# Kernel tuning notes

Measured on AMD Instinct MI355X. Metric: run time of the kernel, lower is better.

## Reference

```python
import jax, jax.numpy as jnp
import numpy as np

LOG100 = float(np.log(100.0))
EPS = 1e-12  # F.normalize eps


def _l2norm(x):
    # torch.nn.functional.normalize(x, dim=-1): x / max(||x||_2, eps)
    n = jnp.sqrt(jnp.sum(x * x, axis=-1, keepdims=True))
    return x / jnp.maximum(n, EPS)


def setup_inputs() -> dict:
    key = jax.random.key(0)
    k1, k2, k3, k4, k5 = jax.random.split(key, 5)
    B_, nH, N, d = 256, 8, 256, 64
    q = jax.random.normal(k1, (B_, nH, N, d), dtype=jnp.float32)
    k = jax.random.normal(k2, (B_, nH, N, d), dtype=jnp.float32)
    v = jax.random.normal(k3, (B_, nH, N, d), dtype=jnp.float32)
    logit_scale = jax.random.normal(k4, (nH, 1, 1), dtype=jnp.float32)
    bias = jax.random.normal(k5, (nH, N, N), dtype=jnp.float32)
    return {"q": q, "k": k, "v": v, "logit_scale": logit_scale, "bias": bias}


def reference(q, k, v, logit_scale, bias):
    B_, nH, N, d = q.shape
    # cosine-similarity attention (euclidean_dist=False branch)
    scores = jnp.einsum("bhnd,bhmd->bhnm", _l2norm(q), _l2norm(k))
    # attn_transform: Swin-v2-style clamped learned logit scale + rel-pos bias
    scale = jnp.exp(jnp.minimum(logit_scale, LOG100))  # (nH,1,1)
    scores = scores * scale[None] + bias[None]
    attn = jax.nn.softmax(scores, axis=-1)
    # attn_drop with p=0 is identity
    x = jnp.einsum("bhnm,bhmd->bhnd", attn, v)
    # reshape=True branch: x.transpose(1,2).reshape(B_, -1, H*head_dim) with H==N
    x = jnp.transpose(x, (0, 2, 1, 3)).reshape(B_, -1, N * d)  # (B_, nH, N*d)
    return x
```

## Files before the change

kernel.cpp:

```cpp
#include <hip/hip_runtime.h>

#define LOG100 4.605170185988091f
#define LOG2E  1.4426950408889634f

typedef _Float16 half8 __attribute__((ext_vector_type(8)));
typedef float f32x16 __attribute__((ext_vector_type(16)));

__global__ __launch_bounds__(256) void bias_pack(const float* __restrict__ bias,
                                                 unsigned* __restrict__ biasP) {
  __shared__ float tile[32][33];
  const int head = blockIdx.z;
  const int m0 = blockIdx.x * 32;
  const int n0 = blockIdx.y * 32;
  const float* src = bias + head * 65536;
  unsigned* dst = biasP + head * 32768;
  const int tx = threadIdx.x, ty = threadIdx.y;
#pragma unroll
  for (int i = ty; i < 32; i += 8) tile[i][tx] = src[(n0 + i) * 256 + m0 + tx];
  __syncthreads();
#pragma unroll
  for (int j = ty; j < 16; j += 8) {
    const float lo = tile[tx][2 * j] * LOG2E;
    const float hi = tile[tx][2 * j + 1] * LOG2E;
    dst[(m0 / 2 + j) * 256 + n0 + tx] =
        __builtin_bit_cast(unsigned, __builtin_amdgcn_cvt_pkrtz(lo, hi));
  }
}

template <bool USE_BT>
__global__ __launch_bounds__(512, 4) void attn_kernel(
    const float* __restrict__ q, const float* __restrict__ k, const float* __restrict__ v,
    const float* __restrict__ logit_scale, const float* __restrict__ bias,
    const unsigned* __restrict__ biasP, float* __restrict__ out) {
  __shared__ __align__(16) char smem[32768];
  _Float16* Kn = (_Float16*)smem;
  _Float16* Vt = (_Float16*)(smem + 16384);

  const int tid = threadIdx.x;
  const int wave = tid >> 6;
  const int lane = tid & 63;
  const int l31 = lane & 31;
  const int hi = lane >> 5;
  const int head = blockIdx.x;
  const int b = blockIdx.y;

  const long base = ((long)(b * 8 + head)) * (256 * 64);
  const float* qp = q + base;
  const float* kp = k + base;
  const float* vp = v + base;

  const float scale2 = __expf(fminf(logit_scale[head], LOG100)) * LOG2E;

  const int qrow = wave * 32 + l31;
  half8 qfrag[4];
  {
    float qf[4][8];
    float ssq = 0.f;
#pragma unroll
    for (int dk = 0; dk < 4; ++dk) {
      const float4 x0 = *(const float4*)(qp + qrow * 64 + dk * 16 + hi * 8);
      const float4 x1 = *(const float4*)(qp + qrow * 64 + dk * 16 + hi * 8 + 4);
      qf[dk][0] = x0.x; qf[dk][1] = x0.y; qf[dk][2] = x0.z; qf[dk][3] = x0.w;
      qf[dk][4] = x1.x; qf[dk][5] = x1.y; qf[dk][6] = x1.z; qf[dk][7] = x1.w;
      ssq += x0.x * x0.x + x0.y * x0.y + x0.z * x0.z + x0.w * x0.w;
      ssq += x1.x * x1.x + x1.y * x1.y + x1.z * x1.z + x1.w * x1.w;
    }
    ssq += __shfl_xor(ssq, 32);
    const float qinv = rsqrtf(fmaxf(ssq, 1e-24f));
#pragma unroll
    for (int dk = 0; dk < 4; ++dk)
#pragma unroll
      for (int j = 0; j < 8; ++j) qfrag[dk][j] = (_Float16)(qf[dk][j] * qinv);
  }

  f32x16 o0 = {};
  f32x16 o1 = {};
  float m = -1.0e30f, lsum = 0.f;

  const unsigned* bP = USE_BT ? (biasP + head * 32768 + qrow) : nullptr;
  const float* bF = USE_BT ? nullptr : (bias + head * 65536 + qrow * 256 + 4 * hi);

  for (int h = 0; h < 2; ++h) {
    if (h) __syncthreads();

    {
      const int row_in = tid >> 4;
      const int seg = tid & 15;
#pragma unroll
      for (int it = 0; it < 4; ++it) {
        const int r = it * 32 + row_in;
        const float4 a = *(const float4*)(kp + (h * 128 + r) * 64 + seg * 4);
        float ss = a.x * a.x + a.y * a.y + a.z * a.z + a.w * a.w;
        ss += __shfl_xor(ss, 1);
        ss += __shfl_xor(ss, 2);
        ss += __shfl_xor(ss, 4);
        ss += __shfl_xor(ss, 8);
        const float inv = rsqrtf(fmaxf(ss, 1e-24f));
        union { _Float16 hh[4]; uint2 u; } pk4;
        pk4.hh[0] = (_Float16)(a.x * inv);
        pk4.hh[1] = (_Float16)(a.y * inv);
        pk4.hh[2] = (_Float16)(a.z * inv);
        pk4.hh[3] = (_Float16)(a.w * inv);
        char* wp = (char*)Kn + r * 128 + ((seg * 8) ^ ((r & 15) << 3));
        *(uint2*)wp = pk4.u;
      }
    }

    {
      const int r = lane >> 4;
      const int sx = lane & 15;
#pragma unroll
      for (int it = 0; it < 4; ++it) {
        const int kv0 = (wave * 4 + it) * 4;
        float4 a = *(const float4*)(vp + (h * 128 + kv0 + r) * 64 + sx * 4);
        float e1 = (r & 1) ? a.x : a.y;
        float g1 = __shfl_xor(e1, 16);
        float e2 = (r & 1) ? a.z : a.w;
        float g2 = __shfl_xor(e2, 16);
        if (r & 1) { a.x = g1; a.z = g2; } else { a.y = g1; a.w = g2; }
        float e3 = (r & 2) ? a.x : a.z;
        float g3 = __shfl_xor(e3, 32);
        float e4 = (r & 2) ? a.y : a.w;
        float g4 = __shfl_xor(e4, 32);
        if (r & 2) { a.x = g3; a.y = g4; } else { a.z = g3; a.w = g4; }
        const int d = 4 * sx + r;
        union { _Float16 hh[4]; uint2 u; } pk4;
        pk4.hh[0] = (_Float16)a.x;
        pk4.hh[1] = (_Float16)a.y;
        pk4.hh[2] = (_Float16)a.z;
        pk4.hh[3] = (_Float16)a.w;
        char* wp = (char*)Vt + d * 256 + ((kv0 * 2) ^ ((d & 15) << 4));
        *(uint2*)wp = pk4.u;
      }
    }

    __syncthreads();

    for (int c = 0; c < 4; ++c) {
      unsigned bw[8];
      float bvf[16];
      if (USE_BT) {
#pragma unroll
        for (int i = 0; i < 8; ++i) {
          const int kp_off = (i & 1) + 4 * (i >> 1) + 2 * hi;
          bw[i] = bP[(h * 64 + c * 16 + kp_off) * 256];
        }
      } else {
        const int kvg = h * 128 + c * 32;
#pragma unroll
        for (int reg = 0; reg < 16; ++reg) {
          const int kvr = (reg & 3) + 8 * (reg >> 2);
          bvf[reg] = bF[kvg + kvr] * LOG2E;
        }
      }

      const int krow = c * 32 + l31;
      const char* kbase = (const char*)Kn + krow * 128;
      const int kmsk = (krow & 15) << 3;
      f32x16 s = {};
      __builtin_amdgcn_s_setprio(1);
#pragma unroll
      for (int dk = 0; dk < 4; ++dk) {
        union { uint2 u[2]; half8 hh; } kf;
        kf.u[0] = *(const uint2*)(kbase + ((dk * 32 + hi * 16) ^ kmsk));
        kf.u[1] = *(const uint2*)(kbase + ((dk * 32 + hi * 16 + 8) ^ kmsk));
        s = __builtin_amdgcn_mfma_f32_32x32x16_f16(kf.hh, qfrag[dk], s, 0, 0, 0);
      }
      __builtin_amdgcn_s_setprio(0);

      if (USE_BT) {
#pragma unroll
        for (int i = 0; i < 8; ++i) {
          const _Float16* hp = (const _Float16*)&bw[i];
          s[2 * i] = fmaf(s[2 * i], scale2, (float)hp[0]);
          s[2 * i + 1] = fmaf(s[2 * i + 1], scale2, (float)hp[1]);
        }
      } else {
#pragma unroll
        for (int reg = 0; reg < 16; ++reg) s[reg] = fmaf(s[reg], scale2, bvf[reg]);
      }

      float m8[8];
#pragma unroll
      for (int i = 0; i < 8; ++i) m8[i] = fmaxf(s[2 * i], s[2 * i + 1]);
      float m4[4];
#pragma unroll
      for (int i = 0; i < 4; ++i) m4[i] = fmaxf(m8[2 * i], m8[2 * i + 1]);
      float mx = fmaxf(fmaxf(m4[0], m4[1]), fmaxf(m4[2], m4[3]));
      mx = fmaxf(mx, __shfl_xor(mx, 32));

      if (__any(mx > m + 8.0f)) {
        const float mnew = fmaxf(m, mx);
        const float corr = exp2f(m - mnew);
        lsum *= corr;
#pragma unroll
        for (int i = 0; i < 16; ++i) { o0[i] *= corr; o1[i] *= corr; }
        m = mnew;
      }

#pragma unroll
      for (int reg = 0; reg < 16; ++reg) s[reg] = exp2f(s[reg] - m);
      float a8[8];
#pragma unroll
      for (int i = 0; i < 8; ++i) a8[i] = s[2 * i] + s[2 * i + 1];
      float a4[4];
#pragma unroll
      for (int i = 0; i < 4; ++i) a4[i] = a8[2 * i] + a8[2 * i + 1];
      float psum = (a4[0] + a4[1]) + (a4[2] + a4[3]);
      psum += __shfl_xor(psum, 32);
      lsum += psum;

      unsigned pk[8];
#pragma unroll
      for (int i = 0; i < 8; ++i)
        pk[i] = __builtin_bit_cast(unsigned, __builtin_amdgcn_cvt_pkrtz(s[2 * i], s[2 * i + 1]));
      const unsigned ra = __shfl_xor(hi ? pk[0] : pk[2], 32);
      const unsigned rb = __shfl_xor(hi ? pk[1] : pk[3], 32);
      const unsigned rc = __shfl_xor(hi ? pk[4] : pk[6], 32);
      const unsigned rd = __shfl_xor(hi ? pk[5] : pk[7], 32);
      union { unsigned u[4]; half8 hh; } f0, f1;
      f0.u[0] = hi ? ra : pk[0];
      f0.u[1] = hi ? rb : pk[1];
      f0.u[2] = hi ? pk[2] : ra;
      f0.u[3] = hi ? pk[3] : rb;
      f1.u[0] = hi ? rc : pk[4];
      f1.u[1] = hi ? rd : pk[5];
      f1.u[2] = hi ? pk[6] : rc;
      f1.u[3] = hi ? pk[7] : rd;

      {
        const int d = l31;
        const char* vbase = (const char*)Vt + d * 256;
        const int msk = (d & 15) << 4;
        const half8 vf0 = *(const half8*)(vbase + ((c * 64 + hi * 16) ^ msk));
        const half8 vf1 = *(const half8*)(vbase + ((c * 64 + 32 + hi * 16) ^ msk));
        __builtin_amdgcn_s_setprio(1);
        o0 = __builtin_amdgcn_mfma_f32_32x32x16_f16(vf0, f0.hh, o0, 0, 0, 0);
        o0 = __builtin_amdgcn_mfma_f32_32x32x16_f16(vf1, f1.hh, o0, 0, 0, 0);
        __builtin_amdgcn_s_setprio(0);
      }
      {
        const int d = 32 + l31;
        const char* vbase = (const char*)Vt + d * 256;
        const int msk = (d & 15) << 4;
        const half8 vf0 = *(const half8*)(vbase + ((c * 64 + hi * 16) ^ msk));
        const half8 vf1 = *(const half8*)(vbase + ((c * 64 + 32 + hi * 16) ^ msk));
        __builtin_amdgcn_s_setprio(1);
        o1 = __builtin_amdgcn_mfma_f32_32x32x16_f16(vf0, f0.hh, o1, 0, 0, 0);
        o1 = __builtin_amdgcn_mfma_f32_32x32x16_f16(vf1, f1.hh, o1, 0, 0, 0);
        __builtin_amdgcn_s_setprio(0);
      }
    }
  }

  __syncthreads();

  char* ob = (char*)smem + wave * 4096;
  const float invl = 1.0f / lsum;
#pragma unroll
  for (int r = 0; r < 16; r += 2) {
    const int d0 = (r & 3) + 8 * (r >> 2) + 4 * hi;
    const unsigned w0 =
        __builtin_bit_cast(unsigned, __builtin_amdgcn_cvt_pkrtz(o0[r] * invl, o0[r + 1] * invl));
    *(unsigned*)(ob + l31 * 128 + ((d0 * 2) ^ ((l31 & 15) << 3))) = w0;
    const unsigned w1 =
        __builtin_bit_cast(unsigned, __builtin_amdgcn_cvt_pkrtz(o1[r] * invl, o1[r + 1] * invl));
    *(unsigned*)(ob + l31 * 128 + (((d0 + 32) * 2) ^ ((l31 & 15) << 3))) = w1;
  }
  __asm__ __volatile__("s_waitcnt lgkmcnt(0)" ::: "memory");
  __builtin_amdgcn_sched_barrier(0);
  const int sx = lane & 15;
  const int rr = lane >> 4;
#pragma unroll
  for (int kq = 0; kq < 8; ++kq) {
    const int qq = kq * 4 + rr;
    union { uint2 u; _Float16 hh[4]; } rd4;
    rd4.u = *(const uint2*)(ob + qq * 128 + ((sx * 8) ^ ((qq & 15) << 3)));
    float4 val;
    val.x = (float)rd4.hh[0];
    val.y = (float)rd4.hh[1];
    val.z = (float)rd4.hh[2];
    val.w = (float)rd4.hh[3];
    *(float4*)(out + (((long)(b * 256 + wave * 32 + qq) * 8 + head) * 64 + 4 * sx)) = val;
  }
}

extern "C" void kernel_launch(void* const* d_in, const int* in_sizes, int n_in,
                              void* d_out, int out_size, void* d_ws, size_t ws_size,
                              hipStream_t stream) {
  (void)in_sizes; (void)n_in; (void)out_size;
  const float* q = (const float*)d_in[0];
  const float* k = (const float*)d_in[1];
  const float* v = (const float*)d_in[2];
  const float* ls = (const float*)d_in[3];
  const float* bias = (const float*)d_in[4];
  float* out = (float*)d_out;
  const size_t bpBytes = (size_t)8 * 128 * 256 * 4;
  if (ws_size >= bpBytes) {
    unsigned* biasP = (unsigned*)d_ws;
    bias_pack<<<dim3(8, 8, 8), dim3(32, 8), 0, stream>>>(bias, biasP);
    attn_kernel<true><<<dim3(8, 256), dim3(512), 0, stream>>>(q, k, v, ls, bias, biasP, out);
  } else {
    attn_kernel<false><<<dim3(8, 256), dim3(512), 0, stream>>>(q, k, v, ls, bias, nullptr, out);
  }
}
```

Measured before the change: 176.7 us.

## Stage full K/V in LDS once and software-pipeline QK^T with softmax-PV

Instead of staging K and V in two 128-row halves with a barrier between them, the kernel now normalizes and stages all 256 rows of K and the transposed V into a 64 KB shared buffer up front, with new XOR swizzles and 128-bit K fragment loads. The chunk loop is then unrolled and software-pipelined so the QK^T MFMA for the next chunk is issued before the softmax and PV work of the current chunk. This removes a barrier and the setprio hints and lets MFMA overlap VALU work. In exchange it doubles LDS per block (occupancy at 512 threads may drop) and raises register pressure from holding two score tiles.

```diff
diff --git a/kernel.cpp b/kernel.cpp
--- a/kernel.cpp
+++ b/kernel.cpp
@@ -32,9 +32,9 @@
     const float* __restrict__ q, const float* __restrict__ k, const float* __restrict__ v,
     const float* __restrict__ logit_scale, const float* __restrict__ bias,
     const unsigned* __restrict__ biasP, float* __restrict__ out) {
-  __shared__ __align__(16) char smem[32768];
+  __shared__ __align__(16) char smem[65536];
   _Float16* Kn = (_Float16*)smem;
-  _Float16* Vt = (_Float16*)(smem + 16384);
+  _Float16* Vt = (_Float16*)(smem + 32768);
 
   const int tid = threadIdx.x;
   const int wave = tid >> 6;
@@ -73,6 +73,59 @@
       for (int j = 0; j < 8; ++j) qfrag[dk][j] = (_Float16)(qf[dk][j] * qinv);
   }
 
+  {
+    const int row_in = tid >> 4;
+    const int seg = tid & 15;
+#pragma unroll
+    for (int it = 0; it < 8; ++it) {
+      const int row = it * 32 + row_in;
+      const float4 a = *(const float4*)(kp + row * 64 + seg * 4);
+      float ss = a.x * a.x + a.y * a.y + a.z * a.z + a.w * a.w;
+      ss += __shfl_xor(ss, 1);
+      ss += __shfl_xor(ss, 2);
+      ss += __shfl_xor(ss, 4);
+      ss += __shfl_xor(ss, 8);
+      const float inv = rsqrtf(fmaxf(ss, 1e-24f));
+      union { _Float16 hh[4]; uint2 u; } pk4;
+      pk4.hh[0] = (_Float16)(a.x * inv);
+      pk4.hh[1] = (_Float16)(a.y * inv);
+      pk4.hh[2] = (_Float16)(a.z * inv);
+      pk4.hh[3] = (_Float16)(a.w * inv);
+      char* wp = (char*)Kn + row * 128 + ((seg * 8) ^ ((row & 7) << 4));
+      *(uint2*)wp = pk4.u;
+    }
+  }
+
+  {
+    const int r = lane >> 4;
+    const int sx = lane & 15;
+#pragma unroll
+    for (int it = 0; it < 8; ++it) {
+      const int kv0 = (wave * 8 + it) * 4;
+      float4 a = *(const float4*)(vp + (kv0 + r) * 64 + sx * 4);
+      float e1 = (r & 1) ? a.x : a.y;
+      float g1 = __shfl_xor(e1, 16);
+      float e2 = (r & 1) ? a.z : a.w;
+      float g2 = __shfl_xor(e2, 16);
+      if (r & 1) { a.x = g1; a.z = g2; } else { a.y = g1; a.w = g2; }
+      float e3 = (r & 2) ? a.x : a.z;
+      float g3 = __shfl_xor(e3, 32);
+      float e4 = (r & 2) ? a.y : a.w;
+      float g4 = __shfl_xor(e4, 32);
+      if (r & 2) { a.x = g3; a.y = g4; } else { a.z = g3; a.w = g4; }
+      const int d = 4 * sx + r;
+      union { _Float16 hh[4]; uint2 u; } pk4;
+      pk4.hh[0] = (_Float16)a.x;
+      pk4.hh[1] = (_Float16)a.y;
+      pk4.hh[2] = (_Float16)a.z;
+      pk4.hh[3] = (_Float16)a.w;
+      char* wp = (char*)Vt + d * 512 + ((kv0 * 2) ^ ((d & 31) << 4));
+      *(uint2*)wp = pk4.u;
+    }
+  }
+
+  __syncthreads();
+
   f32x16 o0 = {};
   f32x16 o1 = {};
   float m = -1.0e30f, lsum = 0.f;
@@ -80,177 +133,123 @@
   const unsigned* bP = USE_BT ? (biasP + head * 32768 + qrow) : nullptr;
   const float* bF = USE_BT ? nullptr : (bias + head * 65536 + qrow * 256 + 4 * hi);
 
-  for (int h = 0; h < 2; ++h) {
-    if (h) __syncthreads();
-
+  auto LOADB = [&](int c, unsigned bw[8]) {
+    if (USE_BT) {
+#pragma unroll
+      for (int i = 0; i < 8; ++i) {
+        const int kp_off = (i & 1) + 4 * (i >> 1) + 2 * hi;
+        bw[i] = bP[(c * 16 + kp_off) * 256];
+      }
+    } else {
+#pragma unroll
+      for (int i = 0; i < 8; ++i) {
+        const int kvr0 = 2 * ((i & 1) + 4 * (i >> 1) + 2 * hi);
+        const float lo = bF[c * 32 + kvr0 - 4 * hi + ((kvr0 & 7) >= 4 ? 0 : 0)] * LOG2E;
+        const float l0 = bF[c * 32 + ((2 * i) & 3) + 8 * ((2 * i) >> 2)] * LOG2E;
+        const float l1 = bF[c * 32 + ((2 * i + 1) & 3) + 8 * ((2 * i + 1) >> 2)] * LOG2E;
+        bw[i] = __builtin_bit_cast(unsigned, __builtin_amdgcn_cvt_pkrtz(l0, l1));
+        (void)lo; (void)kvr0;
+      }
+    }
+  };
+
+  auto QKT = [&](int c) -> f32x16 {
+    const int krow = c * 32 + l31;
+    const char* kbase = (const char*)Kn + krow * 128;
+    const int kmsk = (krow & 7) << 4;
+    f32x16 s = {};
+#pragma unroll
+    for (int dk = 0; dk < 4; ++dk) {
+      const half8 kf = *(const half8*)(kbase + ((dk * 32 + hi * 16) ^ kmsk));
+      s = __builtin_amdgcn_mfma_f32_32x32x16_f16(kf, qfrag[dk], s, 0, 0, 0);
+    }
+    return s;
+  };
+
+  auto SOFTPV = [&](f32x16 s, int c, const unsigned bw[8]) {
+#pragma unroll
+    for (int i = 0; i < 8; ++i) {
+      const _Float16* hp = (const _Float16*)&bw[i];
+      s[2 * i] = fmaf(s[2 * i], scale2, (float)hp[0]);
+      s[2 * i + 1] = fmaf(s[2 * i + 1], scale2, (float)hp[1]);
+    }
+    float m8[8];
+#pragma unroll
+    for (int i = 0; i < 8; ++i) m8[i] = fmaxf(s[2 * i], s[2 * i + 1]);
+    float m4[4];
+#pragma unroll
+    for (int i = 0; i < 4; ++i) m4[i] = fmaxf(m8[2 * i], m8[2 * i + 1]);
+    float mx = fmaxf(fmaxf(m4[0], m4[1]), fmaxf(m4[2], m4[3]));
+    mx = fmaxf(mx, __shfl_xor(mx, 32));
+    if (__any(mx > m + 8.0f)) {
+      const float mnew = fmaxf(m, mx);
+      const float corr = exp2f(m - mnew);
+      lsum *= corr;
+#pragma unroll
+      for (int i = 0; i < 16; ++i) { o0[i] *= corr; o1[i] *= corr; }
+      m = mnew;
+    }
+#pragma unroll
+    for (int reg = 0; reg < 16; ++reg) s[reg] = exp2f(s[reg] - m);
+    float a8[8];
+#pragma unroll
+    for (int i = 0; i < 8; ++i) a8[i] = s[2 * i] + s[2 * i + 1];
+    float a4[4];
+#pragma unroll
+    for (int i = 0; i < 4; ++i) a4[i] = a8[2 * i] + a8[2 * i + 1];
+    float psum = (a4[0] + a4[1]) + (a4[2] + a4[3]);
+    psum += __shfl_xor(psum, 32);
+    lsum += psum;
+    unsigned pk[8];
+#pragma unroll
+    for (int i = 0; i < 8; ++i)
+      pk[i] = __builtin_bit_cast(unsigned, __builtin_amdgcn_cvt_pkrtz(s[2 * i], s[2 * i + 1]));
+    const unsigned ra = __shfl_xor(hi ? pk[0] : pk[2], 32);
+    const unsigned rb = __shfl_xor(hi ? pk[1] : pk[3], 32);
+    const unsigned rc = __shfl_xor(hi ? pk[4] : pk[6], 32);
+    const unsigned rd = __shfl_xor(hi ? pk[5] : pk[7], 32);
+    union { unsigned u[4]; half8 hh; } f0, f1;
+    f0.u[0] = hi ? ra : pk[0];
+    f0.u[1] = hi ? rb : pk[1];
+    f0.u[2] = hi ? pk[2] : ra;
+    f0.u[3] = hi ? pk[3] : rb;
+    f1.u[0] = hi ? rc : pk[4];
+    f1.u[1] = hi ? rd : pk[5];
+    f1.u[2] = hi ? pk[6] : rc;
+    f1.u[3] = hi ? pk[7] : rd;
     {
-      const int row_in = tid >> 4;
-      const int seg = tid & 15;
-#pragma unroll
-      for (int it = 0; it < 4; ++it) {
-        const int r = it * 32 + row_in;
-        const float4 a = *(const float4*)(kp + (h * 128 + r) * 64 + seg * 4);
-        float ss = a.x * a.x + a.y * a.y + a.z * a.z + a.w * a.w;
-        ss += __shfl_xor(ss, 1);
-        ss += __shfl_xor(ss, 2);
-        ss += __shfl_xor(ss, 4);
-        ss += __shfl_xor(ss, 8);
-        const float inv = rsqrtf(fmaxf(ss, 1e-24f));
-        union { _Float16 hh[4]; uint2 u; } pk4;
-        pk4.hh[0] = (_Float16)(a.x * inv);
-        pk4.hh[1] = (_Float16)(a.y * inv);
-        pk4.hh[2] = (_Float16)(a.z * inv);
-        pk4.hh[3] = (_Float16)(a.w * inv);
-        char* wp = (char*)Kn + r * 128 + ((seg * 8) ^ ((r & 15) << 3));
-        *(uint2*)wp = pk4.u;
-      }
-    }
-
+      const int d = l31;
+      const char* vbase = (const char*)Vt + d * 512;
+      const int msk = (d & 31) << 4;
+      const half8 vf0 = *(const half8*)(vbase + ((c * 64 + hi * 16) ^ msk));
+      const half8 vf1 = *(const half8*)(vbase + ((c * 64 + 32 + hi * 16) ^ msk));
+      o0 = __builtin_amdgcn_mfma_f32_32x32x16_f16(vf0, f0.hh, o0, 0, 0, 0);
+      o0 = __builtin_amdgcn_mfma_f32_32x32x16_f16(vf1, f1.hh, o0, 0, 0, 0);
+    }
     {
-      const int r = lane >> 4;
-      const int sx = lane & 15;
-#pragma unroll
-      for (int it = 0; it < 4; ++it) {
-        const int kv0 = (wave * 4 + it) * 4;
-        float4 a = *(const float4*)(vp + (h * 128 + kv0 + r) * 64 + sx * 4);
-        float e1 = (r & 1) ? a.x : a.y;
-        float g1 = __shfl_xor(e1, 16);
-        float e2 = (r & 1) ? a.z : a.w;
-        float g2 = __shfl_xor(e2, 16);
-        if (r & 1) { a.x = g1; a.z = g2; } else { a.y = g1; a.w = g2; }
-        float e3 = (r & 2) ? a.x : a.z;
-        float g3 = __shfl_xor(e3, 32);
-        float e4 = (r & 2) ? a.y : a.w;
-        float g4 = __shfl_xor(e4, 32);
-        if (r & 2) { a.x = g3; a.y = g4; } else { a.z = g3; a.w = g4; }
-        const int d = 4 * sx + r;
-        union { _Float16 hh[4]; uint2 u; } pk4;
-        pk4.hh[0] = (_Float16)a.x;
-        pk4.hh[1] = (_Float16)a.y;
-        pk4.hh[2] = (_Float16)a.z;
-        pk4.hh[3] = (_Float16)a.w;
-        char* wp = (char*)Vt + d * 256 + ((kv0 * 2) ^ ((d & 15) << 4));
-        *(uint2*)wp = pk4.u;
-      }
-    }
-
-    __syncthreads();
-
-    for (int c = 0; c < 4; ++c) {
-      unsigned bw[8];
-      float bvf[16];
-      if (USE_BT) {
-#pragma unroll
-        for (int i = 0; i < 8; ++i) {
-          const int kp_off = (i & 1) + 4 * (i >> 1) + 2 * hi;
-          bw[i] = bP[(h * 64 + c * 16 + kp_off) * 256];
-        }
-      } else {
-        const int kvg = h * 128 + c * 32;
-#pragma unroll
-        for (int reg = 0; reg < 16; ++reg) {
-          const int kvr = (reg & 3) + 8 * (reg >> 2);
-          bvf[reg] = bF[kvg + kvr] * LOG2E;
-        }
-      }
-
-      const int krow = c * 32 + l31;
-      const char* kbase = (const char*)Kn + krow * 128;
-      const int kmsk = (krow & 15) << 3;
-      f32x16 s = {};
-      __builtin_amdgcn_s_setprio(1);
-#pragma unroll
-      for (int dk = 0; dk < 4; ++dk) {
-        union { uint2 u[2]; half8 hh; } kf;
-        kf.u[0] = *(const uint2*)(kbase + ((dk * 32 + hi * 16) ^ kmsk));
-        kf.u[1] = *(const uint2*)(kbase + ((dk * 32 + hi * 16 + 8) ^ kmsk));
-        s = __builtin_amdgcn_mfma_f32_32x32x16_f16(kf.hh, qfrag[dk], s, 0, 0, 0);
-      }
-      __builtin_amdgcn_s_setprio(0);
-
-      if (USE_BT) {
-#pragma unroll
-        for (int i = 0; i < 8; ++i) {
-          const _Float16* hp = (const _Float16*)&bw[i];
-          s[2 * i] = fmaf(s[2 * i], scale2, (float)hp[0]);
-          s[2 * i + 1] = fmaf(s[2 * i + 1], scale2, (float)hp[1]);
-        }
-      } else {
-#pragma unroll
-        for (int reg = 0; reg < 16; ++reg) s[reg] = fmaf(s[reg], scale2, bvf[reg]);
-      }
-
-      float m8[8];
-#pragma unroll
-      for (int i = 0; i < 8; ++i) m8[i] = fmaxf(s[2 * i], s[2 * i + 1]);
-      float m4[4];
-#pragma unroll
-      for (int i = 0; i < 4; ++i) m4[i] = fmaxf(m8[2 * i], m8[2 * i + 1]);
-      float mx = fmaxf(fmaxf(m4[0], m4[1]), fmaxf(m4[2], m4[3]));
-      mx = fmaxf(mx, __shfl_xor(mx, 32));
-
-      if (__any(mx > m + 8.0f)) {
-        const float mnew = fmaxf(m, mx);
-        const float corr = exp2f(m - mnew);
-        lsum *= corr;
-#pragma unroll
-        for (int i = 0; i < 16; ++i) { o0[i] *= corr; o1[i] *= corr; }
-        m = mnew;
-      }
-
-#pragma unroll
-      for (int reg = 0; reg < 16; ++reg) s[reg] = exp2f(s[reg] - m);
-      float a8[8];
-#pragma unroll
-      for (int i = 0; i < 8; ++i) a8[i] = s[2 * i] + s[2 * i + 1];
-      float a4[4];
-#pragma unroll
-      for (int i = 0; i < 4; ++i) a4[i] = a8[2 * i] + a8[2 * i + 1];
-      float psum = (a4[0] + a4[1]) + (a4[2] + a4[3]);
-      psum += __shfl_xor(psum, 32);
-      lsum += psum;
-
-      unsigned pk[8];
-#pragma unroll
-      for (int i = 0; i < 8; ++i)
-        pk[i] = __builtin_bit_cast(unsigned, __builtin_amdgcn_cvt_pkrtz(s[2 * i], s[2 * i + 1]));
-      const unsigned ra = __shfl_xor(hi ? pk[0] : pk[2], 32);
-      const unsigned rb = __shfl_xor(hi ? pk[1] : pk[3], 32);
-      const unsigned rc = __shfl_xor(hi ? pk[4] : pk[6], 32);
-      const unsigned rd = __shfl_xor(hi ? pk[5] : pk[7], 32);
-      union { unsigned u[4]; half8 hh; } f0, f1;
-      f0.u[0] = hi ? ra : pk[0];
-      f0.u[1] = hi ? rb : pk[1];
-      f0.u[2] = hi ? pk[2] : ra;
-      f0.u[3] = hi ? pk[3] : rb;
-      f1.u[0] = hi ? rc : pk[4];
-      f1.u[1] = hi ? rd : pk[5];
-      f1.u[2] = hi ? pk[6] : rc;
-      f1.u[3] = hi ? pk[7] : rd;
-
-      {
-        const int d = l31;
-        const char* vbase = (const char*)Vt + d * 256;
-        const int msk = (d & 15) << 4;
-        const half8 vf0 = *(const half8*)(vbase + ((c * 64 + hi * 16) ^ msk));
-        const half8 vf1 = *(const half8*)(vbase + ((c * 64 + 32 + hi * 16) ^ msk));
-        __builtin_amdgcn_s_setprio(1);
-        o0 = __builtin_amdgcn_mfma_f32_32x32x16_f16(vf0, f0.hh, o0, 0, 0, 0);
-        o0 = __builtin_amdgcn_mfma_f32_32x32x16_f16(vf1, f1.hh, o0, 0, 0, 0);
-        __builtin_amdgcn_s_setprio(0);
-      }
-      {
-        const int d = 32 + l31;
-        const char* vbase = (const char*)Vt + d * 256;
-        const int msk = (d & 15) << 4;
-        const half8 vf0 = *(const half8*)(vbase + ((c * 64 + hi * 16) ^ msk));
-        const half8 vf1 = *(const half8*)(vbase + ((c * 64 + 32 + hi * 16) ^ msk));
-        __builtin_amdgcn_s_setprio(1);
-        o1 = __builtin_amdgcn_mfma_f32_32x32x16_f16(vf0, f0.hh, o1, 0, 0, 0);
-        o1 = __builtin_amdgcn_mfma_f32_32x32x16_f16(vf1, f1.hh, o1, 0, 0, 0);
-        __builtin_amdgcn_s_setprio(0);
-      }
-    }
+      const int d = 32 + l31;
+      const char* vbase = (const char*)Vt + d * 512;
+      const int msk = (d & 31) << 4;
+      const half8 vf0 = *(const half8*)(vbase + ((c * 64 + hi * 16) ^ msk));
+      const half8 vf1 = *(const half8*)(vbase + ((c * 64 + 32 + hi * 16) ^ msk));
+      o1 = __builtin_amdgcn_mfma_f32_32x32x16_f16(vf0, f0.hh, o1, 0, 0, 0);
+      o1 = __builtin_amdgcn_mfma_f32_32x32x16_f16(vf1, f1.hh, o1, 0, 0, 0);
+    }
+  };
+
+  unsigned bwA[8], bwB[8];
+  LOADB(0, bwA);
+  f32x16 sA = QKT(0);
+#pragma unroll
+  for (int cc = 0; cc < 4; ++cc) {
+    LOADB(2 * cc + 1, bwB);
+    f32x16 sB = QKT(2 * cc + 1);
+    SOFTPV(sA, 2 * cc, bwA);
+    if (cc < 3) {
+      LOADB(2 * cc + 2, bwA);
+      sA = QKT(2 * cc + 2);
+    }
+    SOFTPV(sB, 2 * cc + 1, bwB);
   }
 
   __syncthreads();
```

New measurement: 146.4 us. 1.21x faster.

## Switch to 16x16x32 MFMA tiles with 16 waves and full-sequence K/V staging

Applied to the files above, without the earlier changes.

Each block now runs 1024 threads (16 waves), and each wave owns 16 query rows using 16x16x32 MFMA instead of 32x32x16. All 256 K and V rows are staged into 64KB of shared memory in one pass, which removes the two-half loop and its extra barrier. The goal is more waves to hide latency and lower register pressure per wave. In exchange, shared memory use doubles, which can limit how many blocks fit per CU, and each wave issues more, smaller MFMAs per key chunk.

```diff
diff --git a/kernel.cpp b/kernel.cpp
--- a/kernel.cpp
+++ b/kernel.cpp
@@ -4,7 +4,7 @@
 #define LOG2E  1.4426950408889634f
 
 typedef _Float16 half8 __attribute__((ext_vector_type(8)));
-typedef float f32x16 __attribute__((ext_vector_type(16)));
+typedef float f32x4 __attribute__((ext_vector_type(4)));
 
 __global__ __launch_bounds__(256) void bias_pack(const float* __restrict__ bias,
                                                  unsigned* __restrict__ biasP) {
@@ -28,19 +28,19 @@
 }
 
 template <bool USE_BT>
-__global__ __launch_bounds__(512, 4) void attn_kernel(
+__global__ __launch_bounds__(1024, 8) void attn_kernel(
     const float* __restrict__ q, const float* __restrict__ k, const float* __restrict__ v,
     const float* __restrict__ logit_scale, const float* __restrict__ bias,
     const unsigned* __restrict__ biasP, float* __restrict__ out) {
-  __shared__ __align__(16) char smem[32768];
-  _Float16* Kn = (_Float16*)smem;
-  _Float16* Vt = (_Float16*)(smem + 16384);
+  __shared__ __align__(16) char smem[65536];
+  char* KnB = smem;
+  char* VtB = smem + 32768;
 
   const int tid = threadIdx.x;
-  const int wave = tid >> 6;
+  const int wv = tid >> 6;
   const int lane = tid & 63;
-  const int l31 = lane & 31;
-  const int hi = lane >> 5;
+  const int q16 = lane & 15;
+  const int g = lane >> 4;
   const int head = blockIdx.x;
   const int b = blockIdx.y;
 
@@ -50,238 +50,205 @@
   const float* vp = v + base;
 
   const float scale2 = __expf(fminf(logit_scale[head], LOG100)) * LOG2E;
-
-  const int qrow = wave * 32 + l31;
-  half8 qfrag[4];
+  const int qglob = wv * 16 + q16;
+
+  half8 qfrag[2];
   {
-    float qf[4][8];
+    float qf[2][8];
     float ssq = 0.f;
 #pragma unroll
-    for (int dk = 0; dk < 4; ++dk) {
-      const float4 x0 = *(const float4*)(qp + qrow * 64 + dk * 16 + hi * 8);
-      const float4 x1 = *(const float4*)(qp + qrow * 64 + dk * 16 + hi * 8 + 4);
+    for (int dk = 0; dk < 2; ++dk) {
+      const float4 x0 = *(const float4*)(qp + qglob * 64 + dk * 32 + g * 8);
+      const float4 x1 = *(const float4*)(qp + qglob * 64 + dk * 32 + g * 8 + 4);
       qf[dk][0] = x0.x; qf[dk][1] = x0.y; qf[dk][2] = x0.z; qf[dk][3] = x0.w;
       qf[dk][4] = x1.x; qf[dk][5] = x1.y; qf[dk][6] = x1.z; qf[dk][7] = x1.w;
       ssq += x0.x * x0.x + x0.y * x0.y + x0.z * x0.z + x0.w * x0.w;
       ssq += x1.x * x1.x + x1.y * x1.y + x1.z * x1.z + x1.w * x1.w;
     }
+    ssq += __shfl_xor(ssq, 16);
     ssq += __shfl_xor(ssq, 32);
     const float qinv = rsqrtf(fmaxf(ssq, 1e-24f));
 #pragma unroll
-    for (int dk = 0; dk < 4; ++dk)
+    for (int dk = 0; dk < 2; ++dk)
 #pragma unroll
       for (int j = 0; j < 8; ++j) qfrag[dk][j] = (_Float16)(qf[dk][j] * qinv);
   }
 
-  f32x16 o0 = {};
-  f32x16 o1 = {};
+  {
+    const int row_in = tid >> 4;
+    const int seg = tid & 15;
+#pragma unroll
+    for (int it = 0; it < 4; ++it) {
+      const int row = it * 64 + row_in;
+      const float4 a = *(const float4*)(kp + row * 64 + seg * 4);
+      float ss = a.x * a.x + a.y * a.y + a.z * a.z + a.w * a.w;
+      ss += __shfl_xor(ss, 1);
+      ss += __shfl_xor(ss, 2);
+      ss += __shfl_xor(ss, 4);
+      ss += __shfl_xor(ss, 8);
+      const float inv = rsqrtf(fmaxf(ss, 1e-24f));
+      union { _Float16 hh[4]; uint2 u; } pk4;
+      pk4.hh[0] = (_Float16)(a.x * inv);
+      pk4.hh[1] = (_Float16)(a.y * inv);
+      pk4.hh[2] = (_Float16)(a.z * inv);
+      pk4.hh[3] = (_Float16)(a.w * inv);
+      *(uint2*)(KnB + row * 128 + ((seg * 8) ^ ((row & 7) << 4))) = pk4.u;
+    }
+  }
+
+  {
+    const int r = g;
+    const int sx = q16;
+#pragma unroll
+    for (int it = 0; it < 4; ++it) {
+      const int kv0 = (wv * 4 + it) * 4;
+      float4 a = *(const float4*)(vp + (kv0 + r) * 64 + sx * 4);
+      float e1 = (r & 1) ? a.x : a.y;
+      float g1 = __shfl_xor(e1, 16);
+      float e2 = (r & 1) ? a.z : a.w;
+      float g2 = __shfl_xor(e2, 16);
+      if (r & 1) { a.x = g1; a.z = g2; } else { a.y = g1; a.w = g2; }
+      float e3 = (r & 2) ? a.x : a.z;
+      float g3 = __shfl_xor(e3, 32);
+      float e4 = (r & 2) ? a.y : a.w;
+      float g4 = __shfl_xor(e4, 32);
+      if (r & 2) { a.x = g3; a.y = g4; } else { a.z = g3; a.w = g4; }
+      const int d = 4 * sx + r;
+      const int col0 = (kv0 & ~31) + (((kv0 >> 2) & 3) << 3) + (((kv0 >> 4) & 1) << 2);
+      union { _Float16 hh[4]; uint2 u; } pk4;
+      pk4.hh[0] = (_Float16)a.x;
+      pk4.hh[1] = (_Float16)a.y;
+      pk4.hh[2] = (_Float16)a.z;
+      pk4.hh[3] = (_Float16)a.w;
+      *(uint2*)(VtB + d * 512 + ((col0 * 2) ^ ((d & 31) << 4))) = pk4.u;
+    }
+  }
+
+  __syncthreads();
+
+  f32x4 o[4] = {};
   float m = -1.0e30f, lsum = 0.f;
 
-  const unsigned* bP = USE_BT ? (biasP + head * 32768 + qrow) : nullptr;
-  const float* bF = USE_BT ? nullptr : (bias + head * 65536 + qrow * 256 + 4 * hi);
-
-  for (int h = 0; h < 2; ++h) {
-    if (h) __syncthreads();
-
-    {
-      const int row_in = tid >> 4;
-      const int seg = tid & 15;
-#pragma unroll
-      for (int it = 0; it < 4; ++it) {
-        const int r = it * 32 + row_in;
-        const float4 a = *(const float4*)(kp + (h * 128 + r) * 64 + seg * 4);
-        float ss = a.x * a.x + a.y * a.y + a.z * a.z + a.w * a.w;
-        ss += __shfl_xor(ss, 1);
-        ss += __shfl_xor(ss, 2);
-        ss += __shfl_xor(ss, 4);
-        ss += __shfl_xor(ss, 8);
-        const float inv = rsqrtf(fmaxf(ss, 1e-24f));
-        union { _Float16 hh[4]; uint2 u; } pk4;
-        pk4.hh[0] = (_Float16)(a.x * inv);
-        pk4.hh[1] = (_Float16)(a.y * inv);
-        pk4.hh[2] = (_Float16)(a.z * inv);
-        pk4.hh[3] = (_Float16)(a.w * inv);
-        char* wp = (char*)Kn + r * 128 + ((seg * 8) ^ ((r & 15) << 3));
-        *(uint2*)wp = pk4.u;
-      }
-    }
-
-    {
-      const int r = lane >> 4;
-      const int sx = lane & 15;
-#pragma unroll
-      for (int it = 0; it < 4; ++it) {
-        const int kv0 = (wave * 4 + it) * 4;
-        float4 a = *(const float4*)(vp + (h * 128 + kv0 + r) * 64 + sx * 4);
-        float e1 = (r & 1) ? a.x : a.y;
-        float g1 = __shfl_xor(e1, 16);
-        float e2 = (r & 1) ? a.z : a.w;
-        float g2 = __shfl_xor(e2, 16);
-        if (r & 1) { a.x = g1; a.z = g2; } else { a.y = g1; a.w = g2; }
-        float e3 = (r & 2) ? a.x : a.z;
-        float g3 = __shfl_xor(e3, 32);
-        float e4 = (r & 2) ? a.y : a.w;
-        float g4 = __shfl_xor(e4, 32);
-        if (r & 2) { a.x = g3; a.y = g4; } else { a.z = g3; a.w = g4; }
-        const int d = 4 * sx + r;
-        union { _Float16 hh[4]; uint2 u; } pk4;
-        pk4.hh[0] = (_Float16)a.x;
-        pk4.hh[1] = (_Float16)a.y;
-        pk4.hh[2] = (_Float16)a.z;
-        pk4.hh[3] = (_Float16)a.w;
-        char* wp = (char*)Vt + d * 256 + ((kv0 * 2) ^ ((d & 15) << 4));
-        *(uint2*)wp = pk4.u;
-      }
-    }
-
-    __syncthreads();
-
-    for (int c = 0; c < 4; ++c) {
-      unsigned bw[8];
-      float bvf[16];
-      if (USE_BT) {
-#pragma unroll
-        for (int i = 0; i < 8; ++i) {
-          const int kp_off = (i & 1) + 4 * (i >> 1) + 2 * hi;
-          bw[i] = bP[(h * 64 + c * 16 + kp_off) * 256];
+  const unsigned* bP = USE_BT ? (biasP + head * 32768 + qglob) : nullptr;
+  const float* bF = USE_BT ? nullptr : (bias + head * 65536 + qglob * 256);
+
+  for (int c = 0; c < 8; ++c) {
+    unsigned bw[4];
+    float bvf[8];
+    if (USE_BT) {
+#pragma unroll
+      for (int kvt = 0; kvt < 2; ++kvt)
+#pragma unroll
+        for (int p = 0; p < 2; ++p) bw[kvt * 2 + p] = bP[(c * 16 + kvt * 8 + g * 2 + p) * 256];
+    } else {
+#pragma unroll
+      for (int i = 0; i < 8; ++i)
+        bvf[i] = bF[c * 32 + (i >> 2) * 16 + g * 4 + (i & 3)] * LOG2E;
+    }
+
+    const int rk0 = c * 32 + q16;
+    const char* kb0 = KnB + rk0 * 128;
+    const char* kb1 = KnB + (rk0 + 16) * 128;
+    const int sw = (rk0 & 7) << 4;
+    f32x4 s0 = {}, s1 = {};
+#pragma unroll
+    for (int dk = 0; dk < 2; ++dk) {
+      const half8 kf0 = *(const half8*)(kb0 + ((g * 16 + dk * 64) ^ sw));
+      s0 = __builtin_amdgcn_mfma_f32_16x16x32_f16(kf0, qfrag[dk], s0, 0, 0, 0);
+      const half8 kf1 = *(const half8*)(kb1 + ((g * 16 + dk * 64) ^ sw));
+      s1 = __builtin_amdgcn_mfma_f32_16x16x32_f16(kf1, qfrag[dk], s1, 0, 0, 0);
+    }
+
+    float sv[8];
+    if (USE_BT) {
+#pragma unroll
+      for (int kvt = 0; kvt < 2; ++kvt)
+#pragma unroll
+        for (int p = 0; p < 2; ++p) {
+          const _Float16* hp = (const _Float16*)&bw[kvt * 2 + p];
+          const int i = kvt * 4 + 2 * p;
+          const float* sp = (kvt == 0) ? (const float*)&s0 : (const float*)&s1;
+          sv[i] = fmaf(sp[2 * p], scale2, (float)hp[0]);
+          sv[i + 1] = fmaf(sp[2 * p + 1], scale2, (float)hp[1]);
         }
-      } else {
-        const int kvg = h * 128 + c * 32;
-#pragma unroll
-        for (int reg = 0; reg < 16; ++reg) {
-          const int kvr = (reg & 3) + 8 * (reg >> 2);
-          bvf[reg] = bF[kvg + kvr] * LOG2E;
-        }
-      }
-
-      const int krow = c * 32 + l31;
-      const char* kbase = (const char*)Kn + krow * 128;
-      const int kmsk = (krow & 15) << 3;
-      f32x16 s = {};
-      __builtin_amdgcn_s_setprio(1);
-#pragma unroll
-      for (int dk = 0; dk < 4; ++dk) {
-        union { uint2 u[2]; half8 hh; } kf;
-        kf.u[0] = *(const uint2*)(kbase + ((dk * 32 + hi * 16) ^ kmsk));
-        kf.u[1] = *(const uint2*)(kbase + ((dk * 32 + hi * 16 + 8) ^ kmsk));
-        s = __builtin_amdgcn_mfma_f32_32x32x16_f16(kf.hh, qfrag[dk], s, 0, 0, 0);
-      }
-      __builtin_amdgcn_s_setprio(0);
-
-      if (USE_BT) {
-#pragma unroll
-        for (int i = 0; i < 8; ++i) {
-          const _Float16* hp = (const _Float16*)&bw[i];
-          s[2 * i] = fmaf(s[2 * i], scale2, (float)hp[0]);
-          s[2 * i + 1] = fmaf(s[2 * i + 1], scale2, (float)hp[1]);
-        }
-      } else {
-#pragma unroll
-        for (int reg = 0; reg < 16; ++reg) s[reg] = fmaf(s[reg], scale2, bvf[reg]);
-      }
-
-      float m8[8];
-#pragma unroll
-      for (int i = 0; i < 8; ++i) m8[i] = fmaxf(s[2 * i], s[2 * i + 1]);
-      float m4[4];
-#pragma unroll
-      for (int i = 0; i < 4; ++i) m4[i] = fmaxf(m8[2 * i], m8[2 * i + 1]);
-      float mx = fmaxf(fmaxf(m4[0], m4[1]), fmaxf(m4[2], m4[3]));
-      mx = fmaxf(mx, __shfl_xor(mx, 32));
-
-      if (__any(mx > m + 8.0f)) {
-        const float mnew = fmaxf(m, mx);
-        const float corr = exp2f(m - mnew);
-        lsum *= corr;
-#pragma unroll
-        for (int i = 0; i < 16; ++i) { o0[i] *= corr; o1[i] *= corr; }
-        m = mnew;
-      }
-
-#pragma unroll
-      for (int reg = 0; reg < 16; ++reg) s[reg] = exp2f(s[reg] - m);
-      float a8[8];
-#pragma unroll
-      for (int i = 0; i < 8; ++i) a8[i] = s[2 * i] + s[2 * i + 1];
-      float a4[4];
-#pragma unroll
-      for (int i = 0; i < 4; ++i) a4[i] = a8[2 * i] + a8[2 * i + 1];
-      float psum = (a4[0] + a4[1]) + (a4[2] + a4[3]);
-      psum += __shfl_xor(psum, 32);
-      lsum += psum;
-
-      unsigned pk[8];
-#pragma unroll
-      for (int i = 0; i < 8; ++i)
-        pk[i] = __builtin_bit_cast(unsigned, __builtin_amdgcn_cvt_pkrtz(s[2 * i], s[2 * i + 1]));
-      const unsigned ra = __shfl_xor(hi ? pk[0] : pk[2], 32);
-      const unsigned rb = __shfl_xor(hi ? pk[1] : pk[3], 32);
-      const unsigned rc = __shfl_xor(hi ? pk[4] : pk[6], 32);
-      const unsigned rd = __shfl_xor(hi ? pk[5] : pk[7], 32);
-      union { unsigned u[4]; half8 hh; } f0, f1;
-      f0.u[0] = hi ? ra : pk[0];
-      f0.u[1] = hi ? rb : pk[1];
-      f0.u[2] = hi ? pk[2] : ra;
-      f0.u[3] = hi ? pk[3] : rb;
-      f1.u[0] = hi ? rc : pk[4];
-      f1.u[1] = hi ? rd : pk[5];
-      f1.u[2] = hi ? pk[6] : rc;
-      f1.u[3] = hi ? pk[7] : rd;
-
-      {
-        const int d = l31;
-        const char* vbase = (const char*)Vt + d * 256;
-        const int msk = (d & 15) << 4;
-        const half8 vf0 = *(const half8*)(vbase + ((c * 64 + hi * 16) ^ msk));
-        const half8 vf1 = *(const half8*)(vbase + ((c * 64 + 32 + hi * 16) ^ msk));
-        __builtin_amdgcn_s_setprio(1);
-        o0 = __builtin_amdgcn_mfma_f32_32x32x16_f16(vf0, f0.hh, o0, 0, 0, 0);
-        o0 = __builtin_amdgcn_mfma_f32_32x32x16_f16(vf1, f1.hh, o0, 0, 0, 0);
-        __builtin_amdgcn_s_setprio(0);
-      }
-      {
-        const int d = 32 + l31;
-        const char* vbase = (const char*)Vt + d * 256;
-        const int msk = (d & 15) << 4;
-        const half8 vf0 = *(const half8*)(vbase + ((c * 64 + hi * 16) ^ msk));
-        const half8 vf1 = *(const half8*)(vbase + ((c * 64 + 32 + hi * 16) ^ msk));
-        __builtin_amdgcn_s_setprio(1);
-        o1 = __builtin_amdgcn_mfma_f32_32x32x16_f16(vf0, f0.hh, o1, 0, 0, 0);
-        o1 = __builtin_amdgcn_mfma_f32_32x32x16_f16(vf1, f1.hh, o1, 0, 0, 0);
-        __builtin_amdgcn_s_setprio(0);
-      }
+    } else {
+#pragma unroll
+      for (int i = 0; i < 4; ++i) sv[i] = fmaf(s0[i], scale2, bvf[i]);
+#pragma unroll
+      for (int i = 0; i < 4; ++i) sv[4 + i] = fmaf(s1[i], scale2, bvf[4 + i]);
+    }
+
+    float m4[4];
+#pragma unroll
+    for (int i = 0; i < 4; ++i) m4[i] = fmaxf(sv[2 * i], sv[2 * i + 1]);
+    float mx = fmaxf(fmaxf(m4[0], m4[1]), fmaxf(m4[2], m4[3]));
+    mx = fmaxf(mx, __shfl_xor(mx, 16));
+    mx = fmaxf(mx, __shfl_xor(mx, 32));
+
+    if (__any(mx > m + 8.0f)) {
+      const float mnew = fmaxf(m, mx);
+      const float corr = exp2f(m - mnew);
+      lsum *= corr;
+#pragma unroll
+      for (int dt = 0; dt < 4; ++dt)
+#pragma unroll
+        for (int i = 0; i < 4; ++i) o[dt][i] *= corr;
+      m = mnew;
+    }
+
+#pragma unroll
+    for (int i = 0; i < 8; ++i) sv[i] = exp2f(sv[i] - m);
+    float a4[4];
+#pragma unroll
+    for (int i = 0; i < 4; ++i) a4[i] = sv[2 * i] + sv[2 * i + 1];
+    float psum = (a4[0] + a4[1]) + (a4[2] + a4[3]);
+    psum += __shfl_xor(psum, 16);
+    psum += __shfl_xor(psum, 32);
+    lsum += psum;
+
+    union { unsigned u[4]; half8 hh; } pf;
+    pf.u[0] = __builtin_bit_cast(unsigned, __builtin_amdgcn_cvt_pkrtz(sv[0], sv[1]));
+    pf.u[1] = __builtin_bit_cast(unsigned, __builtin_amdgcn_cvt_pkrtz(sv[2], sv[3]));
+    pf.u[2] = __builtin_bit_cast(unsigned, __builtin_amdgcn_cvt_pkrtz(sv[4], sv[5]));
+    pf.u[3] = __builtin_bit_cast(unsigned, __builtin_amdgcn_cvt_pkrtz(sv[6], sv[7]));
+
+#pragma unroll
+    for (int dt = 0; dt < 4; ++dt) {
+      const int d = dt * 16 + q16;
+      const char* vb = VtB + d * 512;
+      const half8 vf = *(const half8*)(vb + ((c * 64 + g * 16) ^ ((d & 31) << 4)));
+      o[dt] = __builtin_amdgcn_mfma_f32_16x16x32_f16(vf, pf.hh, o[dt], 0, 0, 0);
     }
   }
 
   __syncthreads();
 
-  char* ob = (char*)smem + wave * 4096;
+  char* ob = smem + wv * 2048;
   const float invl = 1.0f / lsum;
 #pragma unroll
-  for (int r = 0; r < 16; r += 2) {
-    const int d0 = (r & 3) + 8 * (r >> 2) + 4 * hi;
-    const unsigned w0 =
-        __builtin_bit_cast(unsigned, __builtin_amdgcn_cvt_pkrtz(o0[r] * invl, o0[r + 1] * invl));
-    *(unsigned*)(ob + l31 * 128 + ((d0 * 2) ^ ((l31 & 15) << 3))) = w0;
-    const unsigned w1 =
-        __builtin_bit_cast(unsigned, __builtin_amdgcn_cvt_pkrtz(o1[r] * invl, o1[r + 1] * invl));
-    *(unsigned*)(ob + l31 * 128 + (((d0 + 32) * 2) ^ ((l31 & 15) << 3))) = w1;
+  for (int dt = 0; dt < 4; ++dt) {
+    uint2 w;
+    w.x = __builtin_bit_cast(unsigned,
+        __builtin_amdgcn_cvt_pkrtz(o[dt][0] * invl, o[dt][1] * invl));
+    w.y = __builtin_bit_cast(unsigned,
+        __builtin_amdgcn_cvt_pkrtz(o[dt][2] * invl, o[dt][3] * invl));
+    *(uint2*)(ob + q16 * 128 + ((dt * 32 + g * 8) ^ (q16 << 3))) = w;
   }
   __asm__ __volatile__("s_waitcnt lgkmcnt(0)" ::: "memory");
   __builtin_amdgcn_sched_barrier(0);
-  const int sx = lane & 15;
-  const int rr = lane >> 4;
-#pragma unroll
-  for (int kq = 0; kq < 8; ++kq) {
-    const int qq = kq * 4 + rr;
+  const int qr = lane >> 2;
+  const int fc = lane & 3;
+#pragma unroll
+  for (int it = 0; it < 4; ++it) {
+    const int s4 = fc + it * 4;
     union { uint2 u; _Float16 hh[4]; } rd4;
-    rd4.u = *(const uint2*)(ob + qq * 128 + ((sx * 8) ^ ((qq & 15) << 3)));
+    rd4.u = *(const uint2*)(ob + qr * 128 + ((s4 * 8) ^ (qr << 3)));
     float4 val;
     val.x = (float)rd4.hh[0];
     val.y = (float)rd4.hh[1];
     val.z = (float)rd4.hh[2];
     val.w = (float)rd4.hh[3];
-    *(float4*)(out + (((long)(b * 256 + wave * 32 + qq) * 8 + head) * 64 + 4 * sx)) = val;
+    *(float4*)(out + (((long)(b * 256 + wv * 16 + qr) * 8 + head) * 64 + s4 * 4)) = val;
   }
 }
 
@@ -299,8 +266,8 @@
   if (ws_size >= bpBytes) {
     unsigned* biasP = (unsigned*)d_ws;
     bias_pack<<<dim3(8, 8, 8), dim3(32, 8), 0, stream>>>(bias, biasP);
-    attn_kernel<true><<<dim3(8, 256), dim3(512), 0, stream>>>(q, k, v, ls, bias, biasP, out);
+    attn_kernel<true><<<dim3(8, 256), dim3(1024), 0, stream>>>(q, k, v, ls, bias, biasP, out);
   } else {
-    attn_kernel<false><<<dim3(8, 256), dim3(512), 0, stream>>>(q, k, v, ls, bias, nullptr, out);
+    attn_kernel<false><<<dim3(8, 256), dim3(1024), 0, stream>>>(q, k, v, ls, bias, nullptr, out);
   }
 }
```

After: 150.9 us. 1.17x faster.
